# Performance work log

Measured on AMD Instinct MI355X. Metric: run time of the kernel, lower is better.

The kernel has to match this reference:

```python
import jax, jax.numpy as jnp
import numpy as np

N_HEADS = 16

def setup_inputs() -> dict:
    key = jax.random.key(0)
    ks = jax.random.split(key, 4)
    B, T, C = 2, 2048, 1024
    scale = 0.02
    return {
        "x": jax.random.normal(ks[0], (B, T, C), dtype=jnp.float32),
        "w_qkv": jax.random.normal(ks[1], (C, 3 * C), dtype=jnp.float32) * scale,
        "b_qkv": jnp.zeros((3 * C,), dtype=jnp.float32),
        "w_out": jax.random.normal(ks[2], (C, C), dtype=jnp.float32) * scale,
        "b_out": jnp.zeros((C,), dtype=jnp.float32),
    }

def reference(x, w_qkv, b_qkv, w_out, b_out):
    B, T, C = x.shape
    H = N_HEADS
    hd = C // H
    qkv = x @ w_qkv + b_qkv                      # [B,T,3C]
    q, k, v = jnp.split(qkv, 3, axis=-1)
    # [B,H,T,hd]
    q = q.reshape(B, T, H, hd).transpose(0, 2, 1, 3)
    k = k.reshape(B, T, H, hd).transpose(0, 2, 1, 3)
    v = v.reshape(B, T, H, hd).transpose(0, 2, 1, 3)
    att = jnp.einsum('bhqd,bhkd->bhqk', q, k) / jnp.sqrt(jnp.float32(hd))
    causal = jnp.tril(jnp.ones((T, T), dtype=bool))
    att = jnp.where(causal, att, -jnp.inf)
    att = jax.nn.softmax(att, axis=-1)
    # dropout is identity in eval mode (p effectively 0 for reference)
    y = jnp.einsum('bhqk,bhkd->bhqd', att, v)
    y = y.transpose(0, 2, 1, 3).reshape(B, T, C)
    return y @ w_out + b_out
```

## Files before the change

kernel.cpp:

```cpp
#include <hip/hip_runtime.h>
#include <hip/hip_bf16.h>

#define DEVI __device__ __forceinline__

typedef __attribute__((ext_vector_type(8))) short bf16x8_t;
typedef __attribute__((ext_vector_type(4))) float f32x4_t;
typedef __attribute__((ext_vector_type(4))) short s16x4_t;
typedef __attribute__((ext_vector_type(2))) unsigned int u32x2_t;

#define QSCALE 0.18033688011112043f
#define EXP2F(x) __builtin_amdgcn_exp2f(x)

static DEVI unsigned short f2b_bits(float f) {
    unsigned int u = __float_as_uint(f);
    unsigned int r = (u + 0x7fffu + ((u >> 16) & 1u)) >> 16;
    return (unsigned short)r;
}

static DEVI unsigned int cvtpk_bf16(float lo, float hi) {
    unsigned int r;
    asm("v_cvt_pk_bf16_f32 %0, %1, %2" : "=v"(r) : "v"(lo), "v"(hi));
    return r;
}

static DEVI void gload16(const short* g, short* l) {
    __builtin_amdgcn_global_load_lds((const __attribute__((address_space(1))) void*)g,
                                     (__attribute__((address_space(3))) void*)l, 16, 0, 0);
}

#define MEMFENCE asm volatile("" ::: "memory")

__global__ __launch_bounds__(256) void prep_k(const float* __restrict__ x, short* __restrict__ xb,
                                              const float* __restrict__ wqkv, short* __restrict__ wqkvT,
                                              const float* __restrict__ wout, short* __restrict__ woutT) {
    const int bid = blockIdx.x;
    const int tid = threadIdx.x;
    if (bid < 4096) {
        const long i = ((long)bid * 256 + tid) * 4;
        const float4 v = *(const float4*)(x + i);
        s16x4_t o;
        o[0] = (short)f2b_bits(v.x); o[1] = (short)f2b_bits(v.y);
        o[2] = (short)f2b_bits(v.z); o[3] = (short)f2b_bits(v.w);
        *(s16x4_t*)(xb + i) = o;
        return;
    }
    __shared__ float tile[32][33];
    const float* w; short* wT; int K, N, bx, by;
    if (bid < 4096 + 3072) {
        const int rel = bid - 4096;
        w = wqkv; wT = wqkvT; K = 1024; N = 3072; bx = rel % 96; by = rel / 96;
    } else {
        const int rel = bid - 7168;
        w = wout; wT = woutT; K = 1024; N = 1024; bx = rel & 31; by = rel >> 5;
    }
    const int n0 = bx * 32, k0 = by * 32;
    const int tx = tid & 31, ty = tid >> 5;
#pragma unroll
    for (int i = 0; i < 4; ++i)
        tile[ty + 8 * i][tx] = w[(long)(k0 + ty + 8 * i) * N + n0 + tx];
    __syncthreads();
#pragma unroll
    for (int i = 0; i < 4; ++i)
        wT[(long)(n0 + ty + 8 * i) * K + k0 + tx] = (short)f2b_bits(tile[tx][ty + 8 * i]);
}

template<int MODE, int NF>
__global__ __launch_bounds__(256, 3) void gemm_bt(const short* __restrict__ A,
                                                  const short* __restrict__ Bt,
                                                  const float* __restrict__ bias,
                                                  void* __restrict__ Cv,
                                                  int M, int N, int K) {
    __shared__ __align__(16) short lsA[2][128 * 32];
    __shared__ __align__(16) short lsB[2][32 * NF * 32];
    const int tid = threadIdx.x;
    const int lane = tid & 63;
    const int w = tid >> 6;
    const int wr = w >> 1, wc = w & 1;
    const int l15 = lane & 15, lg = lane >> 4;
    const long m0 = (long)blockIdx.y * 128;
    const long n0 = (long)blockIdx.x * (32 * NF);

    f32x4_t acc[4][NF] = {};

    const int srow = tid >> 2;
    const int scol = (tid & 3) * 8;
    const short* gA = A + (m0 + srow) * (long)K + scol;
    const short* gB = Bt + (n0 + srow) * (long)K + scol;

    auto STAGE = [&](int kt, int bi) {
        gload16(gA + kt,                &lsA[bi][tid * 8]);
        gload16(gA + kt + (long)64 * K, &lsA[bi][tid * 8 + 2048]);
        gload16(gB + kt,                &lsB[bi][tid * 8]);
        if (NF == 4) gload16(gB + kt + (long)64 * K, &lsB[bi][tid * 8 + 2048]);
    };

    const int nt = K >> 5;
    STAGE(0, 0);
    int buf = 0;

    for (int i = 0; i < nt; ++i) {
        if (i + 1 < nt) {
            STAGE((i + 1) << 5, buf ^ 1);
            if (NF == 4) asm volatile("s_waitcnt vmcnt(4)" ::: "memory");
            else         asm volatile("s_waitcnt vmcnt(3)" ::: "memory");
        } else {
            asm volatile("s_waitcnt vmcnt(0)" ::: "memory");
        }
        __builtin_amdgcn_s_barrier();
        MEMFENCE;
        bf16x8_t af[4], bfr[NF];
#pragma unroll
        for (int m = 0; m < 4; ++m)
            af[m] = *(const bf16x8_t*)&lsA[buf][(wr * 64 + m * 16 + l15) * 32 + lg * 8];
#pragma unroll
        for (int n = 0; n < NF; ++n)
            bfr[n] = *(const bf16x8_t*)&lsB[buf][(wc * NF * 16 + n * 16 + l15) * 32 + lg * 8];
#pragma unroll
        for (int m = 0; m < 4; ++m)
#pragma unroll
            for (int n = 0; n < NF; ++n)
                acc[m][n] = __builtin_amdgcn_mfma_f32_16x16x32_bf16(af[m], bfr[n], acc[m][n], 0, 0, 0);
        MEMFENCE;
        __builtin_amdgcn_s_barrier();
        buf ^= 1;
    }

#pragma unroll
    for (int n = 0; n < NF; ++n) {
        const int col = (int)n0 + wc * NF * 16 + n * 16 + l15;
        const float bv = bias[col];
        if (MODE == 1) {
#pragma unroll
            for (int m = 0; m < 4; ++m) {
                const long row = m0 + wr * 64 + m * 16 + lg * 4;
#pragma unroll
                for (int j = 0; j < 4; ++j)
                    ((float*)Cv)[(row + j) * N + col] = acc[m][n][j] + bv;
            }
        } else {
            const float sc = (col < 1024) ? QSCALE : 1.0f;
#pragma unroll
            for (int m = 0; m < 4; ++m) {
                const long row = m0 + wr * 64 + m * 16 + lg * 4;
#pragma unroll
                for (int j = 0; j < 4; ++j)
                    ((short*)Cv)[(row + j) * N + col] = (short)f2b_bits((acc[m][n][j] + bv) * sc);
            }
        }
    }
}

__global__ __launch_bounds__(256) void vtrans(const short* __restrict__ qkv,
                                              short* __restrict__ vt) {
    __shared__ __align__(16) short tile[64][72];
    const int bh = blockIdx.x >> 5, ti = blockIdx.x & 31;
    const int b = bh >> 4, h = bh & 15;
    const int tid = threadIdx.x;
    const int srow = tid >> 3;
    const int scol = (tid & 7) * 8;
#pragma unroll
    for (int p = 0; p < 2; ++p) {
        const int r = srow + 32 * p;
        *(bf16x8_t*)&tile[r][scol] =
            *(const bf16x8_t*)&qkv[((long)b * 2048 + ti * 64 + r) * 3072 + 2048 + h * 64 + scol];
    }
    __syncthreads();
#pragma unroll
    for (int p = 0; p < 2; ++p) {
        const int hd = srow + 32 * p;
        const int tc = scol;
        bf16x8_t v;
#pragma unroll
        for (int i = 0; i < 8; ++i) v[i] = tile[tc + i][hd];
        *(bf16x8_t*)&vt[((long)bh * 64 + hd) * 2048 + ti * 64 + tc] = v;
    }
}

__global__ __launch_bounds__(256, 4) void attn_fwd(const short* __restrict__ qkv,
                                                   const short* __restrict__ vt,
                                                   short* __restrict__ y,
                                                   float* __restrict__ pwO,
                                                   float* __restrict__ pwL) {
    __shared__ __align__(16) short lsK[2][64 * 64];
    __shared__ __align__(16) short lsV[2][64 * 64];
    __shared__ __align__(16) short lsP[4 * 16 * 64];
    const int bid = blockIdx.x;
    const int bh = bid & 31;
    const int pid = bid >> 5;
    int qi, j0, j1, part;
    if (pid < 16) { qi = pid; part = -1; j0 = 0; j1 = qi + 1; }
    else {
        const int k = pid - 16;
        qi = 16 + (k >> 1); part = k & 1;
        const int h0 = (qi + 1) >> 1;
        j0 = part ? h0 : 0;
        j1 = part ? (qi + 1) : h0;
    }
    const int b = bh >> 4, h = bh & 15;
    const int tid = threadIdx.x, w = tid >> 6, lane = tid & 63;
    const int l15 = lane & 15, lg = lane >> 4;
    const int lg4 = lg * 4;
    const int swz = (l15 & 7) << 4;

    const long qrow = (long)qi * 64 + w * 16 + l15;
    const bf16x8_t qf0 = *(const bf16x8_t*)&qkv[((long)b * 2048 + qrow) * 3072 + h * 64 + lg * 8];
    const bf16x8_t qf1 = *(const bf16x8_t*)&qkv[((long)b * 2048 + qrow) * 3072 + h * 64 + 32 + lg * 8];

    const int srow = tid >> 3;
    const int scolb = (tid & 7) * 16;
    const int sc = (scolb ^ ((srow & 7) << 4)) >> 1;
    const short* gK = qkv + ((long)b * 2048 + srow) * 3072 + 1024 + h * 64 + sc;
    const short* gV = vt + ((long)bh * 64 + srow) * 2048 + sc;

    auto STAGE = [&](int jt, int bufi) {
        const short* k0 = gK + (long)jt * 64 * 3072;
        const short* v0 = gV + (long)jt * 64;
        gload16(k0,             &lsK[bufi][tid * 8]);
        gload16(k0 + 32 * 3072, &lsK[bufi][tid * 8 + 2048]);
        gload16(v0,             &lsV[bufi][tid * 8]);
        gload16(v0 + 32 * 2048, &lsV[bufi][tid * 8 + 2048]);
    };

    float lrow = 0.f;
    f32x4_t oacc[4] = {};

    STAGE(j0, 0);
    int buf = 0;

    char* Pb = (char*)lsP + w * 2048 + l15 * 128;

    for (int j = j0; j < j1; ++j) {
        if (j + 1 < j1) {
            STAGE(j + 1, buf ^ 1);
            asm volatile("s_waitcnt vmcnt(4)" ::: "memory");
        } else {
            asm volatile("s_waitcnt vmcnt(0)" ::: "memory");
        }
        __builtin_amdgcn_s_barrier();
        MEMFENCE;

        const bool diag = (j == qi);
        const char* Kb = (const char*)lsK[buf];
        const char* Vb = (const char*)lsV[buf];

        f32x4_t s[4] = {};
        const int nlim = diag ? (w + 1) : 4;
        __builtin_amdgcn_s_setprio(1);
#pragma unroll
        for (int kq = 0; kq < 2; ++kq) {
            const bf16x8_t qf = kq ? qf1 : qf0;
#pragma unroll
            for (int n = 0; n < 4; ++n) {
                if (n < nlim) {
                    bf16x8_t kf = *(const bf16x8_t*)(Kb + (n * 16 + l15) * 128 + ((kq * 64 + lg * 16) ^ swz));
                    s[n] = __builtin_amdgcn_mfma_f32_16x16x32_bf16(kf, qf, s[n], 0, 0, 0);
                }
            }
        }
        __builtin_amdgcn_s_setprio(0);

        float p[4][4];
#pragma unroll
        for (int n = 0; n < 4; ++n)
#pragma unroll
            for (int r = 0; r < 4; ++r) p[n][r] = s[n][r];

        if (diag) {
            const int ql = w * 16 + l15 - lg4;
#pragma unroll
            for (int n = 0; n < 4; ++n)
#pragma unroll
                for (int r = 0; r < 4; ++r)
                    if (n * 16 + r > ql) p[n][r] = -3e38f;
        }

        float lsum = 0.f;
#pragma unroll
        for (int n = 0; n < 4; ++n) {
#pragma unroll
            for (int r = 0; r < 4; ++r) {
                p[n][r] = EXP2F(p[n][r]);
                lsum += p[n][r];
            }
            u32x2_t dw;
            dw[0] = cvtpk_bf16(p[n][0], p[n][1]);
            dw[1] = cvtpk_bf16(p[n][2], p[n][3]);
            *(u32x2_t*)(Pb + ((n * 32 + lg * 8) ^ swz)) = dw;
        }
        lsum += __shfl_xor(lsum, 16);
        lsum += __shfl_xor(lsum, 32);
        lrow += lsum;

        asm volatile("s_waitcnt lgkmcnt(0)" ::: "memory");

        __builtin_amdgcn_s_setprio(1);
#pragma unroll
        for (int kk = 0; kk < 2; ++kk) {
            if (!(diag && kk * 32 > w * 16 + 15)) {
                bf16x8_t pf = *(const bf16x8_t*)(Pb + ((kk * 64 + lg * 16) ^ swz));
#pragma unroll
                for (int n = 0; n < 4; ++n) {
                    bf16x8_t vf = *(const bf16x8_t*)(Vb + (n * 16 + l15) * 128 + ((kk * 64 + lg * 16) ^ swz));
                    oacc[n] = __builtin_amdgcn_mfma_f32_16x16x32_bf16(pf, vf, oacc[n], 0, 0, 0);
                }
            }
        }
        __builtin_amdgcn_s_setprio(0);
        MEMFENCE;
        __builtin_amdgcn_s_barrier();
        buf ^= 1;
    }

    if (part < 0) {
        float lr[4];
#pragma unroll
        for (int r = 0; r < 4; ++r) lr[r] = 1.0f / __shfl(lrow, lg4 + r);
#pragma unroll
        for (int n = 0; n < 4; ++n)
#pragma unroll
            for (int r = 0; r < 4; ++r) {
                const float ov = oacc[n][r] * lr[r];
                y[((long)b * 2048 + qi * 64 + w * 16 + lg4 + r) * 1024 + h * 64 + n * 16 + l15] =
                    (short)f2b_bits(ov);
            }
    } else {
        float* po = pwO + ((size_t)(part * 32 + bh) * 1024 + (qi * 64 + w * 16 - 1024)) * 64;
#pragma unroll
        for (int n = 0; n < 4; ++n)
#pragma unroll
            for (int r = 0; r < 4; ++r)
                po[(lg4 + r) * 64 + n * 16 + l15] = oacc[n][r];
        if (lg == 0)
            pwL[(size_t)(part * 32 + bh) * 1024 + (qi * 64 + w * 16 + l15 - 1024)] = lrow;
    }
}

__global__ __launch_bounds__(256) void attn_combine(const float* __restrict__ pwO,
                                                    const float* __restrict__ pwL,
                                                    short* __restrict__ y) {
    const int idx = blockIdx.x * 256 + threadIdx.x;
    const int d = idx & 63;
    const int rr = idx >> 6;
    const int bh = rr >> 10, qr = rr & 1023;
    const int b = bh >> 4, h = bh & 15;
    const float l = pwL[rr] + pwL[32768 + rr];
    const float o = pwO[(size_t)rr * 64 + d] + pwO[((size_t)rr + 32768) * 64 + d];
    y[((long)b * 2048 + 1024 + qr) * 1024 + h * 64 + d] = (short)f2b_bits(o / l);
}

extern "C" void kernel_launch(void* const* d_in, const int* in_sizes, int n_in,
                              void* d_out, int out_size, void* d_ws, size_t ws_size,
                              hipStream_t stream) {
    const float* x     = (const float*)d_in[0];
    const float* w_qkv = (const float*)d_in[1];
    const float* b_qkv = (const float*)d_in[2];
    const float* w_out = (const float*)d_in[3];
    const float* b_out = (const float*)d_in[4];

    char* ws = (char*)d_ws;
    short* xb    = (short*)(ws);
    short* vt    = xb;
    short* wqkvT = (short*)(ws + (8u << 20));
    short* woutT = (short*)(ws + (14u << 20));
    short* qkvb  = (short*)(ws + (16u << 20));
    short* yatt  = (short*)(ws + (40u << 20));
    float* pwO   = (float*)(ws + (48u << 20));
    float* pwL   = (float*)(ws + (64u << 20));

    prep_k<<<8192, 256, 0, stream>>>(x, xb, w_qkv, wqkvT, w_out, woutT);
    gemm_bt<0, 4><<<dim3(24, 32), 256, 0, stream>>>(xb, wqkvT, b_qkv, (void*)qkvb, 4096, 3072, 1024);
    vtrans<<<1024, 256, 0, stream>>>(qkvb, vt);
    attn_fwd<<<1536, 256, 0, stream>>>(qkvb, vt, yatt, pwO, pwL);
    attn_combine<<<8192, 256, 0, stream>>>(pwO, pwL, yatt);
    gemm_bt<1, 2><<<dim3(16, 32), 256, 0, stream>>>(yatt, woutT, b_out, d_out, 4096, 1024, 1024);
}
```

Baseline: 190.6 us.

## Fuse V transpose into QKV GEMM epilogue and use 128-row attention blocks

The QKV GEMM epilogue now writes the V columns straight into a transposed per-head layout, so the separate vtrans kernel and its extra pass over memory go away. The attention kernel moves to 512-thread blocks that each cover 128 query rows with 8 waves. Every K/V tile loaded into LDS is therefore shared by twice as many query rows, and per-wave causal masking replaces the diagonal-only logic. The trade-offs are higher LDS and register pressure per block, fewer blocks, and scattered 8-byte stores in the GEMM epilogue for V.

```diff
diff --git a/kernel.cpp b/kernel.cpp
--- a/kernel.cpp
+++ b/kernel.cpp
@@ -69,6 +69,7 @@
                                                   const short* __restrict__ Bt,
                                                   const float* __restrict__ bias,
                                                   void* __restrict__ Cv,
+                                                  short* __restrict__ vtp,
                                                   int M, int N, int K) {
     __shared__ __align__(16) short lsA[2][128 * 32];
     __shared__ __align__(16) short lsB[2][32 * NF * 32];
@@ -137,7 +138,7 @@
                 for (int j = 0; j < 4; ++j)
                     ((float*)Cv)[(row + j) * N + col] = acc[m][n][j] + bv;
             }
-        } else {
+        } else if (col < 2048) {
             const float sc = (col < 1024) ? QSCALE : 1.0f;
 #pragma unroll
             for (int m = 0; m < 4; ++m) {
@@ -146,63 +147,51 @@
                 for (int j = 0; j < 4; ++j)
                     ((short*)Cv)[(row + j) * N + col] = (short)f2b_bits((acc[m][n][j] + bv) * sc);
             }
+        } else {
+            const int hc = col - 2048;
+            const int hh = hc >> 6, dd = hc & 63;
+#pragma unroll
+            for (int m = 0; m < 4; ++m) {
+                const long row = m0 + wr * 64 + m * 16 + lg * 4;
+                const int bb = (int)(row >> 11), tt = (int)(row & 2047);
+                s16x4_t pk;
+#pragma unroll
+                for (int j = 0; j < 4; ++j) pk[j] = (short)f2b_bits(acc[m][n][j] + bv);
+                *(s16x4_t*)&vtp[((long)(bb * 16 + hh) * 64 + dd) * 2048 + tt] = pk;
+            }
         }
     }
 }
 
-__global__ __launch_bounds__(256) void vtrans(const short* __restrict__ qkv,
-                                              short* __restrict__ vt) {
-    __shared__ __align__(16) short tile[64][72];
-    const int bh = blockIdx.x >> 5, ti = blockIdx.x & 31;
-    const int b = bh >> 4, h = bh & 15;
-    const int tid = threadIdx.x;
-    const int srow = tid >> 3;
-    const int scol = (tid & 7) * 8;
-#pragma unroll
-    for (int p = 0; p < 2; ++p) {
-        const int r = srow + 32 * p;
-        *(bf16x8_t*)&tile[r][scol] =
-            *(const bf16x8_t*)&qkv[((long)b * 2048 + ti * 64 + r) * 3072 + 2048 + h * 64 + scol];
-    }
-    __syncthreads();
-#pragma unroll
-    for (int p = 0; p < 2; ++p) {
-        const int hd = srow + 32 * p;
-        const int tc = scol;
-        bf16x8_t v;
-#pragma unroll
-        for (int i = 0; i < 8; ++i) v[i] = tile[tc + i][hd];
-        *(bf16x8_t*)&vt[((long)bh * 64 + hd) * 2048 + ti * 64 + tc] = v;
-    }
-}
-
-__global__ __launch_bounds__(256, 4) void attn_fwd(const short* __restrict__ qkv,
+__global__ __launch_bounds__(512, 6) void attn_fwd(const short* __restrict__ qkv,
                                                    const short* __restrict__ vt,
                                                    short* __restrict__ y,
-                                                   float* __restrict__ pwO,
+                                                   float* __restrict__ pwO0,
+                                                   float* __restrict__ pwO1,
                                                    float* __restrict__ pwL) {
     __shared__ __align__(16) short lsK[2][64 * 64];
     __shared__ __align__(16) short lsV[2][64 * 64];
-    __shared__ __align__(16) short lsP[4 * 16 * 64];
+    __shared__ __align__(16) short lsP[8 * 16 * 64];
     const int bid = blockIdx.x;
     const int bh = bid & 31;
-    const int pid = bid >> 5;
-    int qi, j0, j1, part;
-    if (pid < 16) { qi = pid; part = -1; j0 = 0; j1 = qi + 1; }
+    const int pp = bid >> 5;
+    int qt, j0, j1, part;
+    if (pp < 8) { qt = pp; part = -1; j0 = 0; j1 = 2 * pp + 2; }
     else {
-        const int k = pid - 16;
-        qi = 16 + (k >> 1); part = k & 1;
-        const int h0 = (qi + 1) >> 1;
-        j0 = part ? h0 : 0;
-        j1 = part ? (qi + 1) : h0;
+        const int k = pp - 8;
+        qt = 8 + (k >> 1); part = k & 1;
+        const int half = qt + 1;
+        j0 = part ? half : 0;
+        j1 = part ? (2 * qt + 2) : half;
     }
     const int b = bh >> 4, h = bh & 15;
     const int tid = threadIdx.x, w = tid >> 6, lane = tid & 63;
     const int l15 = lane & 15, lg = lane >> 4;
     const int lg4 = lg * 4;
     const int swz = (l15 & 7) << 4;
-
-    const long qrow = (long)qi * 64 + w * 16 + l15;
+    const int qmin = qt * 128 + w * 16;
+
+    const long qrow = (long)qmin + l15;
     const bf16x8_t qf0 = *(const bf16x8_t*)&qkv[((long)b * 2048 + qrow) * 3072 + h * 64 + lg * 8];
     const bf16x8_t qf1 = *(const bf16x8_t*)&qkv[((long)b * 2048 + qrow) * 3072 + h * 64 + 32 + lg * 8];
 
@@ -213,12 +202,8 @@
     const short* gV = vt + ((long)bh * 64 + srow) * 2048 + sc;
 
     auto STAGE = [&](int jt, int bufi) {
-        const short* k0 = gK + (long)jt * 64 * 3072;
-        const short* v0 = gV + (long)jt * 64;
-        gload16(k0,             &lsK[bufi][tid * 8]);
-        gload16(k0 + 32 * 3072, &lsK[bufi][tid * 8 + 2048]);
-        gload16(v0,             &lsV[bufi][tid * 8]);
-        gload16(v0 + 32 * 2048, &lsV[bufi][tid * 8 + 2048]);
+        gload16(gK + (long)jt * 64 * 3072, &lsK[bufi][tid * 8]);
+        gload16(gV + (long)jt * 64,        &lsV[bufi][tid * 8]);
     };
 
     float lrow = 0.f;
@@ -232,80 +217,88 @@
     for (int j = j0; j < j1; ++j) {
         if (j + 1 < j1) {
             STAGE(j + 1, buf ^ 1);
-            asm volatile("s_waitcnt vmcnt(4)" ::: "memory");
+            asm volatile("s_waitcnt vmcnt(2)" ::: "memory");
         } else {
             asm volatile("s_waitcnt vmcnt(0)" ::: "memory");
         }
         __builtin_amdgcn_s_barrier();
         MEMFENCE;
 
-        const bool diag = (j == qi);
-        const char* Kb = (const char*)lsK[buf];
-        const char* Vb = (const char*)lsV[buf];
-
-        f32x4_t s[4] = {};
-        const int nlim = diag ? (w + 1) : 4;
-        __builtin_amdgcn_s_setprio(1);
-#pragma unroll
-        for (int kq = 0; kq < 2; ++kq) {
-            const bf16x8_t qf = kq ? qf1 : qf0;
+        const int base0 = qmin - j * 64;
+        const bool active = (base0 > -16);
+        if (active) {
+            const bool needmask = (base0 < 63);
+            const int nlim = needmask ? min(4, ((base0 + 15) >> 4) + 1) : 4;
+            const char* Kb = (const char*)lsK[buf];
+            const char* Vb = (const char*)lsV[buf];
+
+            f32x4_t s[4] = {};
+            __builtin_amdgcn_s_setprio(1);
+#pragma unroll
+            for (int kq = 0; kq < 2; ++kq) {
+                const bf16x8_t qf = kq ? qf1 : qf0;
+#pragma unroll
+                for (int n = 0; n < 4; ++n) {
+                    if (n < nlim) {
+                        bf16x8_t kf = *(const bf16x8_t*)(Kb + (n * 16 + l15) * 128 + ((kq * 64 + lg * 16) ^ swz));
+                        s[n] = __builtin_amdgcn_mfma_f32_16x16x32_bf16(kf, qf, s[n], 0, 0, 0);
+                    }
+                }
+            }
+            __builtin_amdgcn_s_setprio(0);
+
+            float p[4][4];
+#pragma unroll
+            for (int n = 0; n < 4; ++n)
+#pragma unroll
+                for (int r = 0; r < 4; ++r) p[n][r] = s[n][r];
+
+            if (needmask) {
+                const int qb = base0 + l15;
+#pragma unroll
+                for (int n = 0; n < 4; ++n)
+#pragma unroll
+                    for (int r = 0; r < 4; ++r)
+                        if (n * 16 + lg4 + r > qb) p[n][r] = -3e38f;
+            }
+
+            float lsum = 0.f;
 #pragma unroll
             for (int n = 0; n < 4; ++n) {
+                u32x2_t dw;
                 if (n < nlim) {
-                    bf16x8_t kf = *(const bf16x8_t*)(Kb + (n * 16 + l15) * 128 + ((kq * 64 + lg * 16) ^ swz));
-                    s[n] = __builtin_amdgcn_mfma_f32_16x16x32_bf16(kf, qf, s[n], 0, 0, 0);
+#pragma unroll
+                    for (int r = 0; r < 4; ++r) {
+                        p[n][r] = EXP2F(p[n][r]);
+                        lsum += p[n][r];
+                    }
+                    dw[0] = cvtpk_bf16(p[n][0], p[n][1]);
+                    dw[1] = cvtpk_bf16(p[n][2], p[n][3]);
+                } else {
+                    dw[0] = 0u; dw[1] = 0u;
                 }
-            }
+                *(u32x2_t*)(Pb + ((n * 32 + lg * 8) ^ swz)) = dw;
+            }
+            lsum += __shfl_xor(lsum, 16);
+            lsum += __shfl_xor(lsum, 32);
+            lrow += lsum;
+
+            asm volatile("s_waitcnt lgkmcnt(0)" ::: "memory");
+
+            __builtin_amdgcn_s_setprio(1);
+#pragma unroll
+            for (int kk = 0; kk < 2; ++kk) {
+                if (!(needmask && kk * 32 > base0 + 15)) {
+                    bf16x8_t pf = *(const bf16x8_t*)(Pb + ((kk * 64 + lg * 16) ^ swz));
+#pragma unroll
+                    for (int n = 0; n < 4; ++n) {
+                        bf16x8_t vf = *(const bf16x8_t*)(Vb + (n * 16 + l15) * 128 + ((kk * 64 + lg * 16) ^ swz));
+                        oacc[n] = __builtin_amdgcn_mfma_f32_16x16x32_bf16(pf, vf, oacc[n], 0, 0, 0);
+                    }
+                }
+            }
+            __builtin_amdgcn_s_setprio(0);
         }
-        __builtin_amdgcn_s_setprio(0);
-
-        float p[4][4];
-#pragma unroll
-        for (int n = 0; n < 4; ++n)
-#pragma unroll
-            for (int r = 0; r < 4; ++r) p[n][r] = s[n][r];
-
-        if (diag) {
-            const int ql = w * 16 + l15 - lg4;
-#pragma unroll
-            for (int n = 0; n < 4; ++n)
-#pragma unroll
-                for (int r = 0; r < 4; ++r)
-                    if (n * 16 + r > ql) p[n][r] = -3e38f;
-        }
-
-        float lsum = 0.f;
-#pragma unroll
-        for (int n = 0; n < 4; ++n) {
-#pragma unroll
-            for (int r = 0; r < 4; ++r) {
-                p[n][r] = EXP2F(p[n][r]);
-                lsum += p[n][r];
-            }
-            u32x2_t dw;
-            dw[0] = cvtpk_bf16(p[n][0], p[n][1]);
-            dw[1] = cvtpk_bf16(p[n][2], p[n][3]);
-            *(u32x2_t*)(Pb + ((n * 32 + lg * 8) ^ swz)) = dw;
-        }
-        lsum += __shfl_xor(lsum, 16);
-        lsum += __shfl_xor(lsum, 32);
-        lrow += lsum;
-
-        asm volatile("s_waitcnt lgkmcnt(0)" ::: "memory");
-
-        __builtin_amdgcn_s_setprio(1);
-#pragma unroll
-        for (int kk = 0; kk < 2; ++kk) {
-            if (!(diag && kk * 32 > w * 16 + 15)) {
-                bf16x8_t pf = *(const bf16x8_t*)(Pb + ((kk * 64 + lg * 16) ^ swz));
-#pragma unroll
-                for (int n = 0; n < 4; ++n) {
-                    bf16x8_t vf = *(const bf16x8_t*)(Vb + (n * 16 + l15) * 128 + ((kk * 64 + lg * 16) ^ swz));
-                    oacc[n] = __builtin_amdgcn_mfma_f32_16x16x32_bf16(pf, vf, oacc[n], 0, 0, 0);
-                }
-            }
-        }
-        __builtin_amdgcn_s_setprio(0);
         MEMFENCE;
         __builtin_amdgcn_s_barrier();
         buf ^= 1;
@@ -318,24 +311,23 @@
 #pragma unroll
         for (int n = 0; n < 4; ++n)
 #pragma unroll
-            for (int r = 0; r < 4; ++r) {
-                const float ov = oacc[n][r] * lr[r];
-                y[((long)b * 2048 + qi * 64 + w * 16 + lg4 + r) * 1024 + h * 64 + n * 16 + l15] =
-                    (short)f2b_bits(ov);
-            }
+            for (int r = 0; r < 4; ++r)
+                y[((long)b * 2048 + qmin + lg4 + r) * 1024 + h * 64 + n * 16 + l15] =
+                    (short)f2b_bits(oacc[n][r] * lr[r]);
     } else {
-        float* po = pwO + ((size_t)(part * 32 + bh) * 1024 + (qi * 64 + w * 16 - 1024)) * 64;
+        float* po = (part ? pwO1 : pwO0) + ((size_t)bh * 1024 + (qmin - 1024)) * 64;
 #pragma unroll
         for (int n = 0; n < 4; ++n)
 #pragma unroll
             for (int r = 0; r < 4; ++r)
                 po[(lg4 + r) * 64 + n * 16 + l15] = oacc[n][r];
         if (lg == 0)
-            pwL[(size_t)(part * 32 + bh) * 1024 + (qi * 64 + w * 16 + l15 - 1024)] = lrow;
-    }
-}
-
-__global__ __launch_bounds__(256) void attn_combine(const float* __restrict__ pwO,
+            pwL[(size_t)part * 32768 + bh * 1024 + (qmin + l15 - 1024)] = lrow;
+    }
+}
+
+__global__ __launch_bounds__(256) void attn_combine(const float* __restrict__ pwO0,
+                                                    const float* __restrict__ pwO1,
                                                     const float* __restrict__ pwL,
                                                     short* __restrict__ y) {
     const int idx = blockIdx.x * 256 + threadIdx.x;
@@ -344,7 +336,7 @@
     const int bh = rr >> 10, qr = rr & 1023;
     const int b = bh >> 4, h = bh & 15;
     const float l = pwL[rr] + pwL[32768 + rr];
-    const float o = pwO[(size_t)rr * 64 + d] + pwO[((size_t)rr + 32768) * 64 + d];
+    const float o = pwO0[(size_t)rr * 64 + d] + pwO1[(size_t)rr * 64 + d];
     y[((long)b * 2048 + 1024 + qr) * 1024 + h * 64 + d] = (short)f2b_bits(o / l);
 }
 
@@ -359,18 +351,18 @@
 
     char* ws = (char*)d_ws;
     short* xb    = (short*)(ws);
-    short* vt    = xb;
+    float* pwO0  = (float*)(ws);
     short* wqkvT = (short*)(ws + (8u << 20));
     short* woutT = (short*)(ws + (14u << 20));
     short* qkvb  = (short*)(ws + (16u << 20));
-    short* yatt  = (short*)(ws + (40u << 20));
-    float* pwO   = (float*)(ws + (48u << 20));
+    short* vt    = (short*)(ws + (40u << 20));
+    short* yatt  = (short*)(ws + (48u << 20));
+    float* pwO1  = (float*)(ws + (56u << 20));
     float* pwL   = (float*)(ws + (64u << 20));
 
     prep_k<<<8192, 256, 0, stream>>>(x, xb, w_qkv, wqkvT, w_out, woutT);
-    gemm_bt<0, 4><<<dim3(24, 32), 256, 0, stream>>>(xb, wqkvT, b_qkv, (void*)qkvb, 4096, 3072, 1024);
-    vtrans<<<1024, 256, 0, stream>>>(qkvb, vt);
-    attn_fwd<<<1536, 256, 0, stream>>>(qkvb, vt, yatt, pwO, pwL);
-    attn_combine<<<8192, 256, 0, stream>>>(pwO, pwL, yatt);
-    gemm_bt<1, 2><<<dim3(16, 32), 256, 0, stream>>>(yatt, woutT, b_out, d_out, 4096, 1024, 1024);
-}
+    gemm_bt<0, 4><<<dim3(24, 32), 256, 0, stream>>>(xb, wqkvT, b_qkv, (void*)qkvb, vt, 4096, 3072, 1024);
+    attn_fwd<<<768, 512, 0, stream>>>(qkvb, vt, yatt, pwO0, pwO1, pwL);
+    attn_combine<<<8192, 256, 0, stream>>>(pwO0, pwO1, pwL, yatt);
+    gemm_bt<1, 2><<<dim3(16, 32), 256, 0, stream>>>(yatt, woutT, b_out, d_out, nullptr, 4096, 1024, 1024);
+}
```

After: 180.8 us. 5.2% less time.
